# Kernel tuning notes

Hardware: AMD Instinct MI355X
Metric: run time of the kernel (lower is better)

Reference implementation:

```python
import jax, jax.numpy as jnp
import numpy as np

B, N, NT, ET = 16, 38, 9, 4
NE = N * (N - 1) // 2          # 703 edge-generation steps
R = N + NE                     # repeat_num = 741 masked subgraphs
H = D = 128                    # nhid / nout
L = 12                         # num_flow_layer
EDIM = ET - 1                  # 3 relation types used by RGCN
EPS = 1e-5
TEMP = 0.1                     # straight-through argmax temperature


def _st_dis(x, w1, b1, w2, b2):
    # MLP -> logits -> straight-through one-hot(argmax)
    h = jnp.tanh(x @ w1.T + b1)
    logits = h @ w2.T + b2
    soft = jax.nn.softmax(logits / TEMP, axis=-1)
    hard = jax.nn.one_hot(jnp.argmax(logits, axis=-1), logits.shape[-1], dtype=logits.dtype)
    return soft + jax.lax.stop_gradient(hard - soft)


def _one_hot_add(inputs, shift):
    # (inputs + shift) mod vocab in one-hot space == circular conv via FFT
    out = jnp.fft.ifft(jnp.fft.fft(inputs, axis=-1) * jnp.fft.fft(shift, axis=-1), axis=-1)
    return jnp.real(out).astype(inputs.dtype)


def _gconv(x, adj, w):
    # x: (b, n, f_in), adj: (b, e, n, n), w: (e*f_out, f_in)
    b, n, _ = x.shape
    s = (x @ w.T).reshape(b, n, EDIM, -1)            # (b, n, e, f_out)
    return jnp.einsum('beij,bjeo->bio', adj, s)      # aggregate over relations


def _rgcn(x, adj, emb_w, gc1_w, gc2_w, gc3_w):
    h = x @ emb_w.T
    h = jax.nn.relu(_gconv(h, adj, gc1_w))
    h = jax.nn.relu(_gconv(h, adj, gc2_w))
    return _gconv(h, adj, gc3_w)                     # no relu on last layer


def setup_inputs():
    key = jax.random.key(0)
    ks = jax.random.split(key, 16)
    s = 0.1
    iu, ju = np.triu_indices(N, k=1)                 # canonical edge order (703, 2)
    return {
        'x': jax.random.uniform(ks[0], (B, N, NT), dtype=jnp.float32),
        'adj': jax.random.uniform(ks[1], (B, ET, N, N), dtype=jnp.float32),
        'x_deq': jax.random.normal(ks[2], (B, N, NT), dtype=jnp.float32),
        'adj_deq': jax.random.normal(ks[3], (B, NE, ET), dtype=jnp.float32),
        'mask_node': jax.random.uniform(ks[4], (R, N)) < 0.5,
        'mask_edge': jax.random.uniform(ks[5], (R, N, N)) < 0.5,
        'index_select_edge': jnp.asarray(np.stack([iu, ju], 1), dtype=jnp.int32),
        'emb_w': jax.random.normal(ks[6], (NT, NT), jnp.float32) * s,
        'gc1_w': jax.random.normal(ks[7], (EDIM * H, NT), jnp.float32) * s,
        'gc2_w': jax.random.normal(ks[8], (EDIM * H, H), jnp.float32) * s,
        'gc3_w': jax.random.normal(ks[9], (EDIM * D, H), jnp.float32) * s,
        'bn_gamma': jnp.ones((D,), jnp.float32),
        'bn_beta': jnp.zeros((D,), jnp.float32),
        'node_w1': jax.random.normal(ks[10], (L, H, D), jnp.float32) * s,
        'node_b1': jnp.zeros((L, H), jnp.float32),
        'node_w2': jax.random.normal(ks[11], (L, NT, H), jnp.float32) * s,
        'node_b2': jnp.zeros((L, NT), jnp.float32),
        'edge_w1': jax.random.normal(ks[12], (L, H, 3 * D), jnp.float32) * s,
        'edge_b1': jnp.zeros((L, H), jnp.float32),
        'edge_w2': jax.random.normal(ks[13], (L, ET, H), jnp.float32) * s,
        'edge_b2': jnp.zeros((L, ET), jnp.float32),
    }


def reference(x, adj, x_deq, adj_deq, mask_node, mask_edge, index_select_edge,
              emb_w, gc1_w, gc2_w, gc3_w, bn_gamma, bn_beta,
              node_w1, node_b1, node_w2, node_b2,
              edge_w1, edge_b1, edge_w2, edge_b2):
    adj3 = adj[:, :EDIM]                                              # (B,3,N,N)
    xr = jnp.where(mask_node[None, :, :, None], x[:, None], 0.0)      # (B,R,N,NT)
    ar = jnp.where(mask_edge[None, :, None], adj3[:, None], 0.0)      # (B,R,3,N,N)
    xr = xr.reshape(B * R, N, NT)
    ar = ar.reshape(B * R, EDIM, N, N)
    node_emb = _rgcn(xr, ar, emb_w, gc1_w, gc2_w, gc3_w)              # (B*R,N,D)
    # BatchNorm1d over channels (training-mode batch statistics, biased var)
    m = node_emb.mean(axis=(0, 1))
    v = node_emb.var(axis=(0, 1))
    node_emb = (node_emb - m) * jax.lax.rsqrt(v + EPS) * bn_gamma + bn_beta
    node_emb = node_emb.reshape(B, R, N, D)
    graph_emb = node_emb.sum(axis=2)                                  # (B,R,D)
    graph_emb_node = graph_emb[:, :N]                                 # (B,N,D)
    graph_emb_edge = graph_emb[:, N:, None]                           # (B,NE,1,D)
    all_node_emb_edge = node_emb[:, N:]                               # (B,NE,N,D)
    idx = jnp.broadcast_to(index_select_edge[None, :, :, None].astype(jnp.int32), (B, NE, 2, D))
    sel = jnp.take_along_axis(all_node_emb_edge, idx, axis=2)         # (B,NE,2,D)
    graph_node_emb_edge = jnp.concatenate([sel, graph_emb_edge], axis=2).reshape(B, NE, 3 * D)
    xd, ad = x_deq, adj_deq
    for i in range(L):
        nt = _st_dis(graph_emb_node, node_w1[i], node_b1[i], node_w2[i], node_b2[i]).astype(x.dtype)
        xd = _one_hot_add(xd, nt)
        et = _st_dis(graph_node_emb_edge, edge_w1[i], edge_b1[i], edge_w2[i], edge_b2[i]).astype(adj.dtype)
        ad = _one_hot_add(ad, et)
    return (xd, ad)
```

## Files before the change

kernel.cpp:

```cpp
#include <hip/hip_runtime.h>

#define B_   16
#define N_   38
#define NT_  9
#define ET_  4
#define NE_  703
#define R_   741
#define L_   12
#define BR_  11856

__global__ __launch_bounds__(128) void k_sx(const float* __restrict__ x,
                                            const float* __restrict__ emb_w,
                                            const float* __restrict__ gc1_w,
                                            float* __restrict__ sx)
{
  int bn = blockIdx.x;
  int t  = threadIdx.x;
  __shared__ float xr[NT_];
  __shared__ float hx[NT_];
  if (t < NT_) xr[t] = x[bn*NT_ + t];
  __syncthreads();
  if (t < NT_) {
    float s = 0.f;
    #pragma unroll
    for (int u = 0; u < NT_; ++u) s += xr[u] * emb_w[t*NT_ + u];
    hx[t] = s;
  }
  __syncthreads();
  for (int eo = t; eo < 384; eo += 128) {
    float s = 0.f;
    #pragma unroll
    for (int u = 0; u < NT_; ++u) s += hx[u] * gc1_w[eo*NT_ + u];
    sx[bn*384 + eo] = s;
  }
}

__global__ __launch_bounds__(128) void k_wt(const float* __restrict__ gc2_w,
                                            const float* __restrict__ gc3_w,
                                            float* __restrict__ Wt)
{
  int blk   = blockIdx.x;
  int which = blk / 384;
  int rem   = blk - which*384;
  int e     = rem >> 7;
  int k     = rem & 127;
  int o     = threadIdx.x;
  const float* src = which ? gc3_w : gc2_w;
  Wt[(((which*3 + e) << 7) + k)*128 + o] = src[((e << 7) + o)*128 + k];
}

__global__ __launch_bounds__(128) void k_wt2(const float* __restrict__ node_w1,
                                             const float* __restrict__ edge_w1,
                                             float* __restrict__ w1t_e,
                                             float* __restrict__ w1t_n)
{
  int blk = blockIdx.x;
  int o   = threadIdx.x;
  if (blk < 12*384) {
    int l = blk / 384, kk = blk - l*384;
    w1t_e[blk*128 + o] = edge_w1[(l*128 + o)*384 + kk];
  } else {
    int row = blk - 12*384;
    int l = row >> 7, k = row & 127;
    w1t_n[row*128 + o] = node_w1[(l*128 + o)*128 + k];
  }
}

__device__ __forceinline__ void fma4(float4& d, float a, const float4& s) {
  d.x += a*s.x; d.y += a*s.y; d.z += a*s.z; d.w += a*s.w;
}

__device__ __forceinline__ void ldA(const float* __restrict__ adj,
                                    const int* __restrict__ mask_edge,
                                    int b, int r, int e, int tid,
                                    float av[5], float a1v[2])
{
  #pragma unroll
  for (int t = 0; t < 5; ++t) {
    int m = tid + (t << 8);
    float v = 0.f;
    if (m < 1216) {
      int j = m >> 5, slot = m & 31;
      int i = (slot >> 2) + ((slot & 3) << 3);
      int   msk = mask_edge[(r*N_ + i)*N_ + j];
      float a   = adj[((b*ET_ + e)*N_ + i)*N_ + j];
      v = msk ? a : 0.f;
    }
    av[t] = v;
  }
  #pragma unroll
  for (int t = 0; t < 2; ++t) {
    int m = tid + (t << 8);
    float v = 0.f;
    if (m < 304) {
      int j = m >> 3;
      int i = (m & 7) + 32;
      if (i < N_) {
        int   msk = mask_edge[(r*N_ + i)*N_ + j];
        float a   = adj[((b*ET_ + e)*N_ + i)*N_ + j];
        v = msk ? a : 0.f;
      }
    }
    a1v[t] = v;
  }
}

__device__ __forceinline__ void stA(float* __restrict__ A4e,
                                    float* __restrict__ A1e, int tid,
                                    const float av[5], const float a1v[2])
{
  #pragma unroll
  for (int t = 0; t < 5; ++t) {
    int m = tid + (t << 8);
    if (m < 1216) A4e[m] = av[t];
  }
  #pragma unroll
  for (int t = 0; t < 2; ++t) {
    int m = tid + (t << 8);
    if (m < 304) A1e[m] = a1v[t];
  }
}

__device__ __forceinline__ void eacc_m(const float* __restrict__ A4e,
                                       const float* __restrict__ A1e,
                                       const float* __restrict__ S_l,
                                       int p, int c,
                                       const int* __restrict__ mn,
                                       float4 d[5])
{
  #pragma unroll 2
  for (int j = 0; j < 38; ++j) {
    if (!mn[j]) continue;
    float4 s4 = *(const float4*)&S_l[(j << 7) + (c << 2)];
    float4 a4 = *(const float4*)&A4e[(j << 5) + (p << 2)];
    float  a1 = A1e[(j << 3) + p];
    fma4(d[0], a4.x, s4); fma4(d[1], a4.y, s4); fma4(d[2], a4.z, s4);
    fma4(d[3], a4.w, s4); fma4(d[4], a1,   s4);
  }
}

__device__ __forceinline__ void eacc_u(const float* __restrict__ A4e,
                                       const float* __restrict__ A1e,
                                       const float* __restrict__ S_l,
                                       int p, int c,
                                       float4 d[5])
{
  #pragma unroll 4
  for (int j = 0; j < 38; ++j) {
    float4 s4 = *(const float4*)&S_l[(j << 7) + (c << 2)];
    float4 a4 = *(const float4*)&A4e[(j << 5) + (p << 2)];
    float  a1 = A1e[(j << 3) + p];
    fma4(d[0], a4.x, s4); fma4(d[1], a4.y, s4); fma4(d[2], a4.z, s4);
    fma4(d[3], a4.w, s4); fma4(d[4], a1,   s4);
  }
}

__device__ __forceinline__ void gemm_fused(const float* __restrict__ H_l,
                                           const float* __restrict__ Wb,
                                           int p, int c, float4 g[3][5])
{
  #pragma unroll
  for (int e = 0; e < 3; ++e)
    #pragma unroll
    for (int q = 0; q < 5; ++q) { g[e][q].x = 0.f; g[e][q].y = 0.f; g[e][q].z = 0.f; g[e][q].w = 0.f; }
  #pragma unroll 1
  for (int k0 = 0; k0 < 128; k0 += 4) {
    float4 h0 = *(const float4*)&H_l[((p+ 0) << 7) + k0];
    float4 h1 = *(const float4*)&H_l[((p+ 8) << 7) + k0];
    float4 h2 = *(const float4*)&H_l[((p+16) << 7) + k0];
    float4 h3 = *(const float4*)&H_l[((p+24) << 7) + k0];
    float4 h4 = *(const float4*)&H_l[((p+32) << 7) + k0];
    #pragma unroll
    for (int e = 0; e < 3; ++e) {
      const float* We = &Wb[(e << 14) + (k0 << 7) + (c << 2)];
      float4 w0 = *(const float4*)&We[  0];
      float4 w1 = *(const float4*)&We[128];
      float4 w2 = *(const float4*)&We[256];
      float4 w3 = *(const float4*)&We[384];
      fma4(g[e][0], h0.x, w0); fma4(g[e][0], h0.y, w1); fma4(g[e][0], h0.z, w2); fma4(g[e][0], h0.w, w3);
      fma4(g[e][1], h1.x, w0); fma4(g[e][1], h1.y, w1); fma4(g[e][1], h1.z, w2); fma4(g[e][1], h1.w, w3);
      fma4(g[e][2], h2.x, w0); fma4(g[e][2], h2.y, w1); fma4(g[e][2], h2.z, w2); fma4(g[e][2], h2.w, w3);
      fma4(g[e][3], h3.x, w0); fma4(g[e][3], h3.y, w1); fma4(g[e][3], h3.z, w2); fma4(g[e][3], h3.w, w3);
      fma4(g[e][4], h4.x, w0); fma4(g[e][4], h4.y, w1); fma4(g[e][4], h4.z, w2); fma4(g[e][4], h4.w, w3);
    }
  }
}

__device__ __forceinline__ void relu_store(float* __restrict__ H_l, int p, int c,
                                           const float4 d[5])
{
  #pragma unroll
  for (int q = 0; q < 5; ++q) {
    float4 t;
    t.x = fmaxf(d[q].x, 0.f); t.y = fmaxf(d[q].y, 0.f);
    t.z = fmaxf(d[q].z, 0.f); t.w = fmaxf(d[q].w, 0.f);
    *(float4*)&H_l[((p + (q << 3)) << 7) + (c << 2)] = t;
  }
}

__global__ __launch_bounds__(256) void k_rgcn(
    const float* __restrict__ adj, const int* __restrict__ mask_node,
    const int* __restrict__ mask_edge, const int* __restrict__ isel,
    const float* __restrict__ sx, const float* __restrict__ Wt,
    float* __restrict__ sumE, float* __restrict__ sumSq,
    float* __restrict__ selw)
{
  const int br  = blockIdx.x;
  const int b   = br / R_;
  const int r   = br - b*R_;
  const int tid = threadIdx.x;
  const int c   = tid & 31;
  const int p   = tid >> 5;

  __shared__ __align__(16) float A4_l[3*1216];
  __shared__ __align__(16) float A1_l[3*304];
  __shared__ __align__(16) float SH_l[40*128];
  __shared__ int mn_l[40];

  if (tid < 40) mn_l[tid] = (tid < 38) ? mask_node[r*N_ + tid] : 0;

  float av[5], a1v[2];
  ldA(adj, mask_edge, b, r, 0, tid, av, a1v);
  __syncthreads();

  float4 d[5];
  #pragma unroll
  for (int q = 0; q < 5; ++q) { d[q].x = d[q].y = d[q].z = d[q].w = 0.f; }

  for (int e = 0; e < 3; ++e) {
    for (int idx = tid; idx < 40*32; idx += 256) {
      int j = idx >> 5, q4 = idx & 31;
      float4 v; v.x = v.y = v.z = v.w = 0.f;
      if (j < N_ && mn_l[j]) v = *(const float4*)&sx[(b*N_ + j)*384 + (e << 7) + (q4 << 2)];
      *(float4*)&SH_l[(j << 7) + (q4 << 2)] = v;
    }
    stA(&A4_l[e*1216], &A1_l[e*304], tid, av, a1v);
    __syncthreads();
    if (e < 2) ldA(adj, mask_edge, b, r, e+1, tid, av, a1v);
    eacc_m(&A4_l[e*1216], &A1_l[e*304], SH_l, p, c, mn_l, d);
    __syncthreads();
  }
  relu_store(SH_l, p, c, d);
  __syncthreads();

  for (int gv = 0; gv < 2; ++gv) {
    float4 g[3][5];
    gemm_fused(SH_l, &Wt[gv*49152], p, c, g);
    #pragma unroll
    for (int q = 0; q < 5; ++q) { d[q].x = d[q].y = d[q].z = d[q].w = 0.f; }
    #pragma unroll
    for (int e = 0; e < 3; ++e) {
      __syncthreads();
      #pragma unroll
      for (int q = 0; q < 5; ++q)
        *(float4*)&SH_l[((p + (q << 3)) << 7) + (c << 2)] = g[e][q];
      __syncthreads();
      eacc_u(&A4_l[e*1216], &A1_l[e*304], SH_l, p, c, d);
    }
    if (gv == 0) {
      __syncthreads();
      relu_store(SH_l, p, c, d);
      __syncthreads();
    }
  }
  __syncthreads();

  {
    float4 sA, sB;
    sA.x = d[0].x+d[1].x+d[2].x+d[3].x+d[4].x;
    sA.y = d[0].y+d[1].y+d[2].y+d[3].y+d[4].y;
    sA.z = d[0].z+d[1].z+d[2].z+d[3].z+d[4].z;
    sA.w = d[0].w+d[1].w+d[2].w+d[3].w+d[4].w;
    sB.x = d[0].x*d[0].x+d[1].x*d[1].x+d[2].x*d[2].x+d[3].x*d[3].x+d[4].x*d[4].x;
    sB.y = d[0].y*d[0].y+d[1].y*d[1].y+d[2].y*d[2].y+d[3].y*d[3].y+d[4].y*d[4].y;
    sB.z = d[0].z*d[0].z+d[1].z*d[1].z+d[2].z*d[2].z+d[3].z*d[3].z+d[4].z*d[4].z;
    sB.w = d[0].w*d[0].w+d[1].w*d[1].w+d[2].w*d[2].w+d[3].w*d[3].w+d[4].w*d[4].w;
    *(float4*)&SH_l[( p      << 7) + (c << 2)] = sA;
    *(float4*)&SH_l[((8 + p) << 7) + (c << 2)] = sB;
  }
  __syncthreads();
  {
    int o = tid & 127, half = tid >> 7;
    float t = 0.f;
    #pragma unroll
    for (int pp = 0; pp < 8; ++pp) t += SH_l[(((half << 3) + pp) << 7) + o];
    if (half == 0) sumE [br*128 + o] = t;
    else           sumSq[br*128 + o] = t;
  }
  if (r >= N_) {
    int k  = r - N_;
    int iu = isel[2*k], ju = isel[2*k+1];
    if (p == (iu & 7)) {
      int mu = iu >> 3;
      float4 v = d[0];
      if (mu == 1) v = d[1]; else if (mu == 2) v = d[2];
      else if (mu == 3) v = d[3]; else if (mu == 4) v = d[4];
      *(float4*)&selw[(((b*NE_ + k)*2 + 0) << 7) + (c << 2)] = v;
    }
    if (p == (ju & 7)) {
      int mu = ju >> 3;
      float4 v = d[0];
      if (mu == 1) v = d[1]; else if (mu == 2) v = d[2];
      else if (mu == 3) v = d[3]; else if (mu == 4) v = d[4];
      *(float4*)&selw[(((b*NE_ + k)*2 + 1) << 7) + (c << 2)] = v;
    }
  }
}

__global__ __launch_bounds__(256) void k_bn1(const float* __restrict__ sumE,
                                             const float* __restrict__ sumSq,
                                             double* __restrict__ part)
{
  int g = blockIdx.x;
  int t = threadIdx.x;
  int o = t & 127, h = t >> 7;
  int lo = g*47;
  int hi = lo + 47; if (hi > BR_) hi = BR_;
  double a1 = 0.0, a2 = 0.0;
  for (int i = lo + h; i < hi; i += 2) {
    a1 += (double)sumE [i*128 + o];
    a2 += (double)sumSq[i*128 + o];
  }
  __shared__ double sh1[256], sh2[256];
  sh1[t] = a1; sh2[t] = a2;
  __syncthreads();
  if (h == 0) {
    part[g*128 + o]           = sh1[o] + sh1[128 + o];
    part[256*128 + g*128 + o] = sh2[o] + sh2[128 + o];
  }
}

__global__ __launch_bounds__(128) void k_bn2(const double* __restrict__ part,
                                             const float* __restrict__ gamma,
                                             const float* __restrict__ beta,
                                             float* __restrict__ bnsc,
                                             float* __restrict__ bnsh)
{
  int o = threadIdx.x;
  double s1 = 0.0, s2 = 0.0;
  for (int g = 0; g < 256; ++g) {
    s1 += part[g*128 + o];
    s2 += part[256*128 + g*128 + o];
  }
  double cnt = (double)BR_ * 38.0;
  double m   = s1 / cnt;
  double var = s2 / cnt - m*m;
  double rs  = 1.0 / sqrt(var + 1e-5);
  double sc  = (double)gamma[o] * rs;
  bnsc[o] = (float)sc;
  bnsh[o] = beta[o] - (float)(m * sc);
}

__global__ __launch_bounds__(128) void k_node(
    const float* __restrict__ sumE, const float* __restrict__ bnsc,
    const float* __restrict__ bnsh,
    const float* __restrict__ w1t_n, const float* __restrict__ b1,
    const float* __restrict__ w2, const float* __restrict__ b2,
    const float* __restrict__ x_deq, float* __restrict__ out)
{
  int blk = blockIdx.x;
  int b   = blk / N_;
  int o   = threadIdx.x;
  __shared__ __align__(16) float xv[128];
  __shared__ __align__(16) float hb[128];
  __shared__ float lg[NT_];
  __shared__ int   P_s;
  int br = b*R_ + (blk - b*N_);
  xv[o] = sumE[br*128 + o]*bnsc[o] + 38.f*bnsh[o];
  if (o == 0) P_s = 0;
  __syncthreads();
  for (int l = 0; l < L_; ++l) {
    const float* wb = &w1t_n[(l << 14)];
    float s = b1[l*128 + o];
    #pragma unroll 2
    for (int k = 0; k < 128; k += 4) {
      float4 x4 = *(const float4*)&xv[k];
      s += wb[((k+0) << 7) + o]*x4.x + wb[((k+1) << 7) + o]*x4.y
         + wb[((k+2) << 7) + o]*x4.z + wb[((k+3) << 7) + o]*x4.w;
    }
    hb[o] = tanhf(s);
    __syncthreads();
    if (o < NT_) {
      const float* w2r = &w2[(l*NT_ + o)*128];
      float s2 = b2[l*NT_ + o];
      for (int k = 0; k < 128; ++k) s2 += w2r[k]*hb[k];
      lg[o] = s2;
    }
    __syncthreads();
    if (o == 0) {
      int best = 0; float bv = lg[0];
      #pragma unroll
      for (int cc = 1; cc < NT_; ++cc) if (lg[cc] > bv) { bv = lg[cc]; best = cc; }
      P_s += best;
    }
    __syncthreads();
  }
  int P = P_s % NT_;
  if (o < NT_) {
    int srcc = o - P; if (srcc < 0) srcc += NT_;
    out[blk*NT_ + o] = x_deq[blk*NT_ + srcc];
  }
}

__global__ __launch_bounds__(256) void k_edge(
    const float* __restrict__ sumE, const float* __restrict__ selw,
    const float* __restrict__ bnsc, const float* __restrict__ bnsh,
    const float* __restrict__ w1t_e, const float* __restrict__ b1,
    const float* __restrict__ w2, const float* __restrict__ b2,
    const float* __restrict__ adj_deq, float* __restrict__ out)
{
  int k = blockIdx.x;
  int t = threadIdx.x;
  int c = t & 31, p = t >> 5;
  __shared__ __align__(16) float xv[16][384];
  __shared__ __align__(16) float hb[16][132];
  __shared__ float lg[16][4];
  __shared__ int   Pf[16];

  for (int idx = t; idx < 16*128; idx += 256) {
    int b = idx >> 7, oo = idx & 127;
    float sc = bnsc[oo], sh = bnsh[oo];
    int base = ((b*NE_ + k)*2)*128;
    xv[b][oo]       = selw[base + oo]      *sc + sh;
    xv[b][128 + oo] = selw[base + 128 + oo]*sc + sh;
    xv[b][256 + oo] = sumE[(b*R_ + N_ + k)*128 + oo]*sc + 38.f*sh;
  }
  int Preg = 0;
  __syncthreads();

  for (int l = 0; l < L_; ++l) {
    float4 acc0, acc1;
    {
      float4 bb4 = *(const float4*)&b1[(l << 7) + (c << 2)];
      acc0 = bb4; acc1 = bb4;
    }
    const float* wl = &w1t_e[(l*384) << 7];
    #pragma unroll 2
    for (int kk = 0; kk < 384; kk += 4) {
      float4 x0 = *(const float4*)&xv[p][kk];
      float4 x1 = *(const float4*)&xv[p + 8][kk];
      const float* wk = wl + (kk << 7) + (c << 2);
      float4 w0 = *(const float4*)&wk[  0];
      float4 w1 = *(const float4*)&wk[128];
      float4 w2v= *(const float4*)&wk[256];
      float4 w3 = *(const float4*)&wk[384];
      fma4(acc0, x0.x, w0); fma4(acc0, x0.y, w1); fma4(acc0, x0.z, w2v); fma4(acc0, x0.w, w3);
      fma4(acc1, x1.x, w0); fma4(acc1, x1.y, w1); fma4(acc1, x1.z, w2v); fma4(acc1, x1.w, w3);
    }
    {
      float4 h;
      h.x = tanhf(acc0.x); h.y = tanhf(acc0.y); h.z = tanhf(acc0.z); h.w = tanhf(acc0.w);
      *(float4*)&hb[p][c << 2] = h;
      h.x = tanhf(acc1.x); h.y = tanhf(acc1.y); h.z = tanhf(acc1.z); h.w = tanhf(acc1.w);
      *(float4*)&hb[p + 8][c << 2] = h;
    }
    __syncthreads();
    if (t < 64) {
      int m = t >> 2, c2 = t & 3;
      const float* w2r = &w2[(l*ET_ + c2)*128];
      float s2 = b2[l*ET_ + c2];
      for (int kk = 0; kk < 128; ++kk) s2 += w2r[kk]*hb[m][kk];
      lg[m][c2] = s2;
    }
    __syncthreads();
    if (t < 16) {
      int best = 0; float bv = lg[t][0];
      #pragma unroll
      for (int cc = 1; cc < ET_; ++cc) if (lg[t][cc] > bv) { bv = lg[t][cc]; best = cc; }
      Preg += best;
    }
    __syncthreads();
  }
  if (t < 16) Pf[t] = Preg & 3;
  __syncthreads();
  if (t < 64) {
    int m = t >> 2, c2 = t & 3;
    int srcc = c2 - Pf[m]; if (srcc < 0) srcc += ET_;
    out[(m*NE_ + k)*ET_ + c2] = adj_deq[(m*NE_ + k)*ET_ + srcc];
  }
}

extern "C" void kernel_launch(void* const* d_in, const int* in_sizes, int n_in,
                              void* d_out, int out_size, void* d_ws, size_t ws_size,
                              hipStream_t stream)
{
  (void)in_sizes; (void)n_in; (void)out_size; (void)ws_size;

  const float* x         = (const float*)d_in[0];
  const float* adj       = (const float*)d_in[1];
  const float* x_deq     = (const float*)d_in[2];
  const float* adj_deq   = (const float*)d_in[3];
  const int*   mask_node = (const int*)d_in[4];
  const int*   mask_edge = (const int*)d_in[5];
  const int*   isel      = (const int*)d_in[6];
  const float* emb_w     = (const float*)d_in[7];
  const float* gc1_w     = (const float*)d_in[8];
  const float* gc2_w     = (const float*)d_in[9];
  const float* gc3_w     = (const float*)d_in[10];
  const float* bn_gamma  = (const float*)d_in[11];
  const float* bn_beta   = (const float*)d_in[12];
  const float* node_w1   = (const float*)d_in[13];
  const float* node_b1   = (const float*)d_in[14];
  const float* node_w2   = (const float*)d_in[15];
  const float* node_b2   = (const float*)d_in[16];
  const float* edge_w1   = (const float*)d_in[17];
  const float* edge_b1   = (const float*)d_in[18];
  const float* edge_w2   = (const float*)d_in[19];
  const float* edge_b2   = (const float*)d_in[20];

  float* out_f = (float*)d_out;

  float*  wsf   = (float*)d_ws;
  float*  sx    = wsf;
  float*  sumE  = sx    + 233472;
  float*  sumSq = sumE  + 1517568;
  float*  selw  = sumSq + 1517568;
  float*  bnsc  = selw  + 2879488;
  float*  bnsh  = bnsc  + 128;
  double* part  = (double*)(bnsh + 128);
  float*  Wt    = (float*)part;
  float*  w1t_e = sumSq;
  float*  w1t_n = sumSq + 589824;

  k_wt  <<<768,      128, 0, stream>>>(gc2_w, gc3_w, Wt);
  k_sx  <<<B_*N_,    128, 0, stream>>>(x, emb_w, gc1_w, sx);
  k_rgcn<<<BR_,      256, 0, stream>>>(adj, mask_node, mask_edge, isel, sx,
                                       Wt, sumE, sumSq, selw);
  k_bn1 <<<256,      256, 0, stream>>>(sumE, sumSq, part);
  k_bn2 <<<1,        128, 0, stream>>>(part, bn_gamma, bn_beta, bnsc, bnsh);
  k_wt2 <<<12*384 + 12*128, 128, 0, stream>>>(node_w1, edge_w1, w1t_e, w1t_n);
  k_node<<<B_*N_,    128, 0, stream>>>(sumE, bnsc, bnsh, w1t_n, node_b1,
                                       node_w2, node_b2, x_deq, out_f);
  k_edge<<<NE_,      256, 0, stream>>>(sumE, selw, bnsc, bnsh, w1t_e, edge_b1,
                                       edge_w2, edge_b2, adj_deq,
                                       out_f + B_*N_*NT_);
}
```

Measured before the change: 2.209 ms.

## Parallelize flow layers across blocks with atomic shift accumulation and final gather

The node and edge MLP kernels previously looped over all 12 flow layers serially inside each block. Because the argmax shifts are independent per layer, each layer now runs in its own block, and the argmax results are summed into integer counters with atomics. A final gather kernel applies the accumulated cyclic shift to the dequantized inputs. The change raises block count twelvefold to fill the GPU, at the cost of reloading the input features per layer plus extra zero and gather launches.

```diff
diff --git a/kernel.cpp b/kernel.cpp
--- a/kernel.cpp
+++ b/kernel.cpp
@@ -307,6 +307,14 @@
   }
 }
 
+__global__ __launch_bounds__(256) void k_zero(int* __restrict__ Pn,
+                                              int* __restrict__ Pe)
+{
+  int i = blockIdx.x*256 + threadIdx.x;
+  if (i < B_*N_)   Pn[i] = 0;
+  if (i < B_*NE_)  Pe[i] = 0;
+}
+
 __global__ __launch_bounds__(256) void k_bn1(const float* __restrict__ sumE,
                                              const float* __restrict__ sumSq,
                                              double* __restrict__ part)
@@ -351,71 +359,64 @@
   bnsh[o] = beta[o] - (float)(m * sc);
 }
 
-__global__ __launch_bounds__(128) void k_node(
+__global__ __launch_bounds__(128) void k_node_par(
     const float* __restrict__ sumE, const float* __restrict__ bnsc,
     const float* __restrict__ bnsh,
     const float* __restrict__ w1t_n, const float* __restrict__ b1,
     const float* __restrict__ w2, const float* __restrict__ b2,
-    const float* __restrict__ x_deq, float* __restrict__ out)
+    int* __restrict__ Pn)
 {
   int blk = blockIdx.x;
-  int b   = blk / N_;
+  int l   = blk / (B_*N_);
+  int bn  = blk - l*(B_*N_);
+  int b   = bn / N_;
   int o   = threadIdx.x;
   __shared__ __align__(16) float xv[128];
   __shared__ __align__(16) float hb[128];
   __shared__ float lg[NT_];
-  __shared__ int   P_s;
-  int br = b*R_ + (blk - b*N_);
+  int br = b*R_ + (bn - b*N_);
   xv[o] = sumE[br*128 + o]*bnsc[o] + 38.f*bnsh[o];
-  if (o == 0) P_s = 0;
-  __syncthreads();
-  for (int l = 0; l < L_; ++l) {
-    const float* wb = &w1t_n[(l << 14)];
-    float s = b1[l*128 + o];
-    #pragma unroll 2
-    for (int k = 0; k < 128; k += 4) {
-      float4 x4 = *(const float4*)&xv[k];
-      s += wb[((k+0) << 7) + o]*x4.x + wb[((k+1) << 7) + o]*x4.y
-         + wb[((k+2) << 7) + o]*x4.z + wb[((k+3) << 7) + o]*x4.w;
-    }
-    hb[o] = tanhf(s);
-    __syncthreads();
-    if (o < NT_) {
-      const float* w2r = &w2[(l*NT_ + o)*128];
-      float s2 = b2[l*NT_ + o];
-      for (int k = 0; k < 128; ++k) s2 += w2r[k]*hb[k];
-      lg[o] = s2;
-    }
-    __syncthreads();
-    if (o == 0) {
-      int best = 0; float bv = lg[0];
-      #pragma unroll
-      for (int cc = 1; cc < NT_; ++cc) if (lg[cc] > bv) { bv = lg[cc]; best = cc; }
-      P_s += best;
-    }
-    __syncthreads();
-  }
-  int P = P_s % NT_;
+  __syncthreads();
+  const float* wb = &w1t_n[l << 14];
+  float s = b1[l*128 + o];
+  #pragma unroll 2
+  for (int k = 0; k < 128; k += 4) {
+    float4 x4 = *(const float4*)&xv[k];
+    s += wb[((k+0) << 7) + o]*x4.x + wb[((k+1) << 7) + o]*x4.y
+       + wb[((k+2) << 7) + o]*x4.z + wb[((k+3) << 7) + o]*x4.w;
+  }
+  hb[o] = tanhf(s);
+  __syncthreads();
   if (o < NT_) {
-    int srcc = o - P; if (srcc < 0) srcc += NT_;
-    out[blk*NT_ + o] = x_deq[blk*NT_ + srcc];
-  }
-}
-
-__global__ __launch_bounds__(256) void k_edge(
+    const float* w2r = &w2[(l*NT_ + o)*128];
+    float s2 = b2[l*NT_ + o];
+    for (int k = 0; k < 128; ++k) s2 += w2r[k]*hb[k];
+    lg[o] = s2;
+  }
+  __syncthreads();
+  if (o == 0) {
+    int best = 0; float bv = lg[0];
+    #pragma unroll
+    for (int cc = 1; cc < NT_; ++cc) if (lg[cc] > bv) { bv = lg[cc]; best = cc; }
+    atomicAdd(&Pn[bn], best);
+  }
+}
+
+__global__ __launch_bounds__(256) void k_edge_par(
     const float* __restrict__ sumE, const float* __restrict__ selw,
     const float* __restrict__ bnsc, const float* __restrict__ bnsh,
     const float* __restrict__ w1t_e, const float* __restrict__ b1,
     const float* __restrict__ w2, const float* __restrict__ b2,
-    const float* __restrict__ adj_deq, float* __restrict__ out)
-{
-  int k = blockIdx.x;
+    int* __restrict__ Pe)
+{
+  int blk = blockIdx.x;
+  int l = blk / NE_;
+  int k = blk - l*NE_;
   int t = threadIdx.x;
   int c = t & 31, p = t >> 5;
   __shared__ __align__(16) float xv[16][384];
   __shared__ __align__(16) float hb[16][132];
   __shared__ float lg[16][4];
-  __shared__ int   Pf[16];
 
   for (int idx = t; idx < 16*128; idx += 256) {
     int b = idx >> 7, oo = idx & 127;
@@ -425,58 +426,69 @@
     xv[b][128 + oo] = selw[base + 128 + oo]*sc + sh;
     xv[b][256 + oo] = sumE[(b*R_ + N_ + k)*128 + oo]*sc + 38.f*sh;
   }
-  int Preg = 0;
-  __syncthreads();
-
-  for (int l = 0; l < L_; ++l) {
-    float4 acc0, acc1;
-    {
-      float4 bb4 = *(const float4*)&b1[(l << 7) + (c << 2)];
-      acc0 = bb4; acc1 = bb4;
-    }
-    const float* wl = &w1t_e[(l*384) << 7];
-    #pragma unroll 2
-    for (int kk = 0; kk < 384; kk += 4) {
-      float4 x0 = *(const float4*)&xv[p][kk];
-      float4 x1 = *(const float4*)&xv[p + 8][kk];
-      const float* wk = wl + (kk << 7) + (c << 2);
-      float4 w0 = *(const float4*)&wk[  0];
-      float4 w1 = *(const float4*)&wk[128];
-      float4 w2v= *(const float4*)&wk[256];
-      float4 w3 = *(const float4*)&wk[384];
-      fma4(acc0, x0.x, w0); fma4(acc0, x0.y, w1); fma4(acc0, x0.z, w2v); fma4(acc0, x0.w, w3);
-      fma4(acc1, x1.x, w0); fma4(acc1, x1.y, w1); fma4(acc1, x1.z, w2v); fma4(acc1, x1.w, w3);
-    }
-    {
-      float4 h;
-      h.x = tanhf(acc0.x); h.y = tanhf(acc0.y); h.z = tanhf(acc0.z); h.w = tanhf(acc0.w);
-      *(float4*)&hb[p][c << 2] = h;
-      h.x = tanhf(acc1.x); h.y = tanhf(acc1.y); h.z = tanhf(acc1.z); h.w = tanhf(acc1.w);
-      *(float4*)&hb[p + 8][c << 2] = h;
-    }
-    __syncthreads();
-    if (t < 64) {
-      int m = t >> 2, c2 = t & 3;
-      const float* w2r = &w2[(l*ET_ + c2)*128];
-      float s2 = b2[l*ET_ + c2];
-      for (int kk = 0; kk < 128; ++kk) s2 += w2r[kk]*hb[m][kk];
-      lg[m][c2] = s2;
-    }
-    __syncthreads();
-    if (t < 16) {
-      int best = 0; float bv = lg[t][0];
-      #pragma unroll
-      for (int cc = 1; cc < ET_; ++cc) if (lg[t][cc] > bv) { bv = lg[t][cc]; best = cc; }
-      Preg += best;
-    }
-    __syncthreads();
-  }
-  if (t < 16) Pf[t] = Preg & 3;
+  __syncthreads();
+
+  float4 acc0, acc1;
+  {
+    float4 bb4 = *(const float4*)&b1[(l << 7) + (c << 2)];
+    acc0 = bb4; acc1 = bb4;
+  }
+  const float* wl = &w1t_e[(l*384) << 7];
+  #pragma unroll 2
+  for (int kk = 0; kk < 384; kk += 4) {
+    float4 x0 = *(const float4*)&xv[p][kk];
+    float4 x1 = *(const float4*)&xv[p + 8][kk];
+    const float* wk = wl + (kk << 7) + (c << 2);
+    float4 w0 = *(const float4*)&wk[  0];
+    float4 w1 = *(const float4*)&wk[128];
+    float4 w2v= *(const float4*)&wk[256];
+    float4 w3 = *(const float4*)&wk[384];
+    fma4(acc0, x0.x, w0); fma4(acc0, x0.y, w1); fma4(acc0, x0.z, w2v); fma4(acc0, x0.w, w3);
+    fma4(acc1, x1.x, w0); fma4(acc1, x1.y, w1); fma4(acc1, x1.z, w2v); fma4(acc1, x1.w, w3);
+  }
+  {
+    float4 h;
+    h.x = tanhf(acc0.x); h.y = tanhf(acc0.y); h.z = tanhf(acc0.z); h.w = tanhf(acc0.w);
+    *(float4*)&hb[p][c << 2] = h;
+    h.x = tanhf(acc1.x); h.y = tanhf(acc1.y); h.z = tanhf(acc1.z); h.w = tanhf(acc1.w);
+    *(float4*)&hb[p + 8][c << 2] = h;
+  }
   __syncthreads();
   if (t < 64) {
     int m = t >> 2, c2 = t & 3;
-    int srcc = c2 - Pf[m]; if (srcc < 0) srcc += ET_;
-    out[(m*NE_ + k)*ET_ + c2] = adj_deq[(m*NE_ + k)*ET_ + srcc];
+    const float* w2r = &w2[(l*ET_ + c2)*128];
+    float s2 = b2[l*ET_ + c2];
+    for (int kk = 0; kk < 128; ++kk) s2 += w2r[kk]*hb[m][kk];
+    lg[m][c2] = s2;
+  }
+  __syncthreads();
+  if (t < 16) {
+    int best = 0; float bv = lg[t][0];
+    #pragma unroll
+    for (int cc = 1; cc < ET_; ++cc) if (lg[t][cc] > bv) { bv = lg[t][cc]; best = cc; }
+    atomicAdd(&Pe[t*NE_ + k], best);
+  }
+}
+
+__global__ __launch_bounds__(64) void k_gather(
+    const int* __restrict__ Pn, const int* __restrict__ Pe,
+    const float* __restrict__ x_deq, const float* __restrict__ adj_deq,
+    float* __restrict__ out)
+{
+  int blk = blockIdx.x;
+  int t   = threadIdx.x;
+  if (blk < B_*N_) {
+    if (t < NT_) {
+      int P = Pn[blk] % NT_;
+      int src = t - P; if (src < 0) src += NT_;
+      out[blk*NT_ + t] = x_deq[blk*NT_ + src];
+    }
+  } else {
+    int k = blk - B_*N_;
+    int m = t >> 2, c2 = t & 3;
+    int P = Pe[m*NE_ + k] & 3;
+    int src = c2 - P; if (src < 0) src += ET_;
+    out[B_*N_*NT_ + (m*NE_ + k)*ET_ + c2] = adj_deq[(m*NE_ + k)*ET_ + src];
   }
 }
 
@@ -521,17 +533,20 @@
   float*  Wt    = (float*)part;
   float*  w1t_e = sumSq;
   float*  w1t_n = sumSq + 589824;
-
-  k_wt  <<<768,      128, 0, stream>>>(gc2_w, gc3_w, Wt);
-  k_sx  <<<B_*N_,    128, 0, stream>>>(x, emb_w, gc1_w, sx);
-  k_rgcn<<<BR_,      256, 0, stream>>>(adj, mask_node, mask_edge, isel, sx,
-                                       Wt, sumE, sumSq, selw);
-  k_bn1 <<<256,      256, 0, stream>>>(sumE, sumSq, part);
-  k_bn2 <<<1,        128, 0, stream>>>(part, bn_gamma, bn_beta, bnsc, bnsh);
-  k_wt2 <<<12*384 + 12*128, 128, 0, stream>>>(node_w1, edge_w1, w1t_e, w1t_n);
-  k_node<<<B_*N_,    128, 0, stream>>>(sumE, bnsc, bnsh, w1t_n, node_b1,
-                                       node_w2, node_b2, x_deq, out_f);
-  k_edge<<<NE_,      256, 0, stream>>>(sumE, selw, bnsc, bnsh, w1t_e, edge_b1,
-                                       edge_w2, edge_b2, adj_deq,
-                                       out_f + B_*N_*NT_);
-}
+  int*    Pn    = (int*)sx;
+  int*    Pe    = Pn + B_*N_;
+
+  k_wt      <<<768,           128, 0, stream>>>(gc2_w, gc3_w, Wt);
+  k_sx      <<<B_*N_,         128, 0, stream>>>(x, emb_w, gc1_w, sx);
+  k_rgcn    <<<BR_,           256, 0, stream>>>(adj, mask_node, mask_edge, isel,
+                                                sx, Wt, sumE, sumSq, selw);
+  k_zero    <<<(B_*NE_ + 255)/256, 256, 0, stream>>>(Pn, Pe);
+  k_bn1     <<<256,           256, 0, stream>>>(sumE, sumSq, part);
+  k_bn2     <<<1,             128, 0, stream>>>(part, bn_gamma, bn_beta, bnsc, bnsh);
+  k_wt2     <<<12*384+12*128, 128, 0, stream>>>(node_w1, edge_w1, w1t_e, w1t_n);
+  k_node_par<<<L_*B_*N_,      128, 0, stream>>>(sumE, bnsc, bnsh, w1t_n, node_b1,
+                                                node_w2, node_b2, Pn);
+  k_edge_par<<<L_*NE_,        256, 0, stream>>>(sumE, selw, bnsc, bnsh, w1t_e,
+                                                edge_b1, edge_w2, edge_b2, Pe);
+  k_gather  <<<B_*N_ + NE_,    64, 0, stream>>>(Pn, Pe, x_deq, adj_deq, out_f);
+}
```

Result: faster. 2.077 ms (-6.0%).
